# Kernel optimization log

Measured on AMD Instinct MI355X. Metric: run time of the kernel, lower is better.

The kernel has to match this reference:

```python
import jax, jax.numpy as jnp
import numpy as np

SHAPE = (32, 512, 512)  # (D, H, W) dense voxel grid
N_ACTIVE = 150000


def setup_inputs() -> dict:
    key = jax.random.key(0)
    k_f, k_w1, k_w2 = jax.random.split(key, 3)
    D, H, W = SHAPE
    # unique active voxel coordinates (collision-free dense-grid hash)
    rng = np.random.default_rng(0)
    lin = rng.permutation(D * H * W)[:N_ACTIVE]
    z = lin // (H * W)
    y = (lin // W) % H
    x = lin % W
    coors = np.stack([np.zeros(N_ACTIVE, np.int32), z.astype(np.int32),
                      y.astype(np.int32), x.astype(np.int32)], axis=1)
    features = jax.random.normal(k_f, (N_ACTIVE, 3), dtype=jnp.float32)
    # per-offset GEMM weights: [K^3, Cin, Cout]
    w1 = jax.random.normal(k_w1, (27, 3, 128), dtype=jnp.float32) * 0.2
    w2 = jax.random.normal(k_w2, (27, 128, 128), dtype=jnp.float32) * 0.05
    return {"features": features, "coors": jnp.asarray(coors), "w1": w1,
            "w2": w2, "batch_size": 1}


def _build_grid(coors):
    D, H, W = SHAPE
    n = coors.shape[0]
    grid = jnp.full((D, H, W), -1, dtype=jnp.int32)
    return grid.at[coors[:, 1], coors[:, 2], coors[:, 3]].set(
        jnp.arange(n, dtype=jnp.int32))


def _subm_conv3d(feat, coors, grid, w):
    """Submanifold 3x3x3 conv: gather active neighbors per offset, GEMM, accumulate.
    feat: [N, Cin]; w: [27, Cin, Cout]; output defined only on active sites -> [N, Cout]."""
    D, H, W = SHAPE
    n = feat.shape[0]
    out = jnp.zeros((n, w.shape[-1]), dtype=feat.dtype)
    k = 0
    for dz in (-1, 0, 1):
        for dy in (-1, 0, 1):
            for dx in (-1, 0, 1):
                nz = coors[:, 1] + dz
                ny = coors[:, 2] + dy
                nx = coors[:, 3] + dx
                inb = ((nz >= 0) & (nz < D) & (ny >= 0) & (ny < H)
                       & (nx >= 0) & (nx < W))
                nidx = grid[jnp.clip(nz, 0, D - 1), jnp.clip(ny, 0, H - 1),
                            jnp.clip(nx, 0, W - 1)]
                valid = inb & (nidx >= 0)
                g = jnp.where(valid[:, None],
                              feat[jnp.clip(nidx, 0, n - 1)], 0.0)  # [N, Cin]
                out = out + g @ w[k]
                k += 1
    return out


def reference(features, coors, w1, w2, batch_size):
    # SparseConvTensor: features [N,3], coors [N,4] (batch,z,y,x), batch_size=1
    grid = _build_grid(coors)
    h = _subm_conv3d(features, coors, grid, w1)   # SubMConv3d(3, 128, 3)
    out = _subm_conv3d(h, coors, grid, w2)        # SubMConv3d(128, 128, 3), shared indice_key
    return out
```

## Files before the change

kernel.cpp:

```cpp
#include <hip/hip_runtime.h>
#include <stdint.h>

#define GD 32
#define GH 512
#define GW 512
#define GDHW (GD * GH * GW)
#define KOFF 27
#define CAP 4096
#define CNTS 32
#define NW2 (KOFF * 128 * 128)

typedef __attribute__((ext_vector_type(8))) short short8;
typedef __attribute__((ext_vector_type(4))) float f32x4;

__device__ __forceinline__ unsigned short f32_to_bf16(float x) {
    unsigned int u = __float_as_uint(x);
    unsigned int r = (u + 0x7FFFu + ((u >> 16) & 1u)) >> 16;
    return (unsigned short)r;
}

__global__ __launch_bounds__(256) void setup_kernel(
    const int* __restrict__ coors, int* __restrict__ grid,
    const float* __restrict__ w2, unsigned short* __restrict__ w2t,
    int* __restrict__ cnts, int n, int nbsc) {
    const int bid = blockIdx.x, t = threadIdx.x;
    if (bid == 0) {
        for (int q = t; q < 26 * CNTS; q += 256) cnts[q] = 0;
    }
    if (bid < nbsc) {
        int i = bid * 256 + t;
        if (i < n) {
            int z = coors[i * 4 + 1];
            int y = coors[i * 4 + 2];
            int x = coors[i * 4 + 3];
            grid[(z * GH + y) * GW + x] = i;
        }
    } else {
        int g = (bid - nbsc) * 256 + t;
        if (g < NW2) {
            int k = g >> 14;
            int c = (g >> 7) & 127;
            int q = g & 127;
            w2t[g] = f32_to_bf16(w2[(k * 128 + q) * 128 + c]);
        }
    }
}

__global__ __launch_bounds__(256) void nbr_kernel(
    const int* __restrict__ coors, const int* __restrict__ grid,
    int* __restrict__ vcnt, int* __restrict__ nbrc,
    int2* __restrict__ pairs, int* __restrict__ cnts, int n) {
    __shared__ int wcnt[4][26];
    __shared__ int kbase[26];

    const int i = blockIdx.x * 256 + threadIdx.x;
    const int t = threadIdx.x, wave = t >> 6, lane = t & 63;
    const bool live = (i < n);
    const unsigned long long lmask = (1ull << lane) - 1;

    int z = 0, y = 0, x = 0;
    if (live) {
        z = coors[i * 4 + 1];
        y = coors[i * 4 + 2];
        x = coors[i * 4 + 3];
    }

    int j[27];
#pragma unroll
    for (int k = 0; k < 27; ++k) {
        if (k == 13) { j[k] = live ? i : -1; continue; }
        int dz = k / 9 - 1, dy = (k / 3) % 3 - 1, dx = k % 3 - 1;
        int nz = z + dz, ny = y + dy, nx = x + dx;
        int cz = min(max(nz, 0), GD - 1);
        int cy = min(max(ny, 0), GH - 1);
        int cx = min(max(nx, 0), GW - 1);
        int jj = grid[(cz * GH + cy) * GW + cx];
        bool ok = live && nz >= 0 && nz < GD && ny >= 0 && ny < GH &&
                  nx >= 0 && nx < GW;
        j[k] = ok ? jj : -1;
    }

    if (live) {
        int c = 0;
#pragma unroll
        for (int k = 0; k < 27; ++k) {
            if (k == 13) continue;
            if (j[k] >= 0) { nbrc[i * 27 + c] = (k << 20) | j[k]; ++c; }
        }
        vcnt[i] = c;
    }

#pragma unroll
    for (int kk = 0; kk < 26; ++kk) {
        const int k = kk + (kk >= 13);
        unsigned long long m = __ballot(live && (j[k] >= 0));
        if (lane == 0) wcnt[wave][kk] = __popcll(m);
    }
    __syncthreads();
    if (t < 26) {
        int tot = wcnt[0][t] + wcnt[1][t] + wcnt[2][t] + wcnt[3][t];
        kbase[t] = (tot > 0) ? atomicAdd(&cnts[t * CNTS], tot) : 0;
    }
    __syncthreads();
#pragma unroll
    for (int kk = 0; kk < 26; ++kk) {
        const int k = kk + (kk >= 13);
        const bool valid = live && (j[k] >= 0);
        unsigned long long m = __ballot(valid);
        if (valid) {
            int off = 0;
#pragma unroll
            for (int w = 0; w < 4; ++w)
                if (w < wave) off += wcnt[w][kk];
            int pos = kbase[kk] + off + __popcll(m & lmask);
            if (pos < CAP) pairs[kk * CAP + pos] = make_int2(i, j[k]);
        }
    }
}

__global__ __launch_bounds__(256) void conv1_kernel(
    const float* __restrict__ feat, const float* __restrict__ w1,
    const int* __restrict__ vcnt, const int* __restrict__ nbrc,
    unsigned short* __restrict__ hout, int n) {
    const int wave = threadIdx.x >> 6, lane = threadIdx.x & 63;
    const int i = blockIdx.x * 4 + wave;
    if (i >= n) return;
    const int c2 = lane * 2;

    const int cnt = vcnt[i];
    float f0 = feat[i * 3 + 0];
    float f1 = feat[i * 3 + 1];
    float f2 = feat[i * 3 + 2];

    const float* wc = w1 + 13 * 384 + c2;
    float2 w0 = *(const float2*)(wc);
    float2 wv1 = *(const float2*)(wc + 128);
    float2 w2_ = *(const float2*)(wc + 256);
    float a0 = f0 * w0.x + f1 * wv1.x + f2 * w2_.x;
    float a1 = f0 * w0.y + f1 * wv1.y + f2 * w2_.y;

    for (int s = 0; s < cnt; ++s) {
        int e = nbrc[i * 27 + s];
        int k = e >> 20, j = e & 0xFFFFF;
        float g0 = feat[j * 3 + 0];
        float g1 = feat[j * 3 + 1];
        float g2 = feat[j * 3 + 2];
        const float* wk = w1 + k * 384 + c2;
        float2 u0 = *(const float2*)(wk);
        float2 u1 = *(const float2*)(wk + 128);
        float2 u2 = *(const float2*)(wk + 256);
        a0 += g0 * u0.x + g1 * u1.x + g2 * u2.x;
        a1 += g0 * u0.y + g1 * u1.y + g2 * u2.y;
    }

    unsigned int packed = (unsigned int)f32_to_bf16(a0) |
                          ((unsigned int)f32_to_bf16(a1) << 16);
    *(unsigned int*)(hout + (size_t)i * 128 + c2) = packed;
}

__global__ __launch_bounds__(256, 2) void conv2a_kernel(
    const unsigned short* __restrict__ h,
    const unsigned short* __restrict__ w2t,
    float* __restrict__ out, int n) {
    const int t = threadIdx.x;
    const int wave = t >> 6, lane = t & 63;
    const int lane16 = lane & 15, quad = lane >> 4;
    const int wm = wave >> 1, wn = wave & 1;
    const int row0 = blockIdx.x * 128;

    short8 a[4][4];
#pragma unroll
    for (int ms = 0; ms < 4; ++ms) {
        int r = row0 + wm * 64 + ms * 16 + lane16;
        r = min(r, n - 1);
        const unsigned short* hp = h + (size_t)r * 128 + quad * 8;
#pragma unroll
        for (int ks = 0; ks < 4; ++ks)
            a[ms][ks] = *(const short8*)(hp + ks * 32);
    }

    short8 b[4][4];
    const unsigned short* wbase = w2t + 13 * 16384 + quad * 8;
#pragma unroll
    for (int ns = 0; ns < 4; ++ns) {
        int c = wn * 64 + ns * 16 + lane16;
        const unsigned short* wp = wbase + c * 128;
#pragma unroll
        for (int ks = 0; ks < 4; ++ks)
            b[ns][ks] = *(const short8*)(wp + ks * 32);
    }

    f32x4 acc[4][4];
#pragma unroll
    for (int p = 0; p < 4; ++p)
#pragma unroll
        for (int q = 0; q < 4; ++q) acc[p][q] = (f32x4){0.f, 0.f, 0.f, 0.f};

#pragma unroll
    for (int ks = 0; ks < 4; ++ks)
#pragma unroll
        for (int ns = 0; ns < 4; ++ns)
#pragma unroll
            for (int ms = 0; ms < 4; ++ms)
                acc[ms][ns] = __builtin_amdgcn_mfma_f32_16x16x32_bf16(
                    a[ms][ks], b[ns][ks], acc[ms][ns], 0, 0, 0);

#pragma unroll
    for (int ms = 0; ms < 4; ++ms) {
#pragma unroll
        for (int r = 0; r < 4; ++r) {
            int i = row0 + wm * 64 + ms * 16 + quad * 4 + r;
            if (i < n) {
#pragma unroll
                for (int ns = 0; ns < 4; ++ns) {
                    int col = wn * 64 + ns * 16 + lane16;
                    out[(size_t)i * 128 + col] = acc[ms][ns][r];
                }
            }
        }
    }
}

__global__ __launch_bounds__(256, 2) void conv2b_kernel(
    const unsigned short* __restrict__ h,
    const unsigned short* __restrict__ w2t,
    const int2* __restrict__ pairs, const int* __restrict__ cnts,
    float* __restrict__ out) {
    const int kb = blockIdx.x >> 5;
    const int tile = blockIdx.x & 31;
    const int cnt = min(cnts[kb * CNTS], CAP);
    const int base = tile * 128;
    if (base >= cnt) return;
    const int m = min(128, cnt - base);
    const int k = kb + (kb >= 13);
    const int2* pk = pairs + kb * CAP + base;

    const int t = threadIdx.x;
    const int wave = t >> 6, lane = t & 63;
    const int lane16 = lane & 15, quad = lane >> 4;
    const int wm = wave >> 1, wn = wave & 1;

    short8 a[4][4];
#pragma unroll
    for (int ms = 0; ms < 4; ++ms) {
        int r = wm * 64 + ms * 16 + lane16;
        bool v = (r < m);
        int j = v ? pk[r].y : 0;
        const unsigned short* hp = h + (size_t)j * 128 + quad * 8;
#pragma unroll
        for (int ks = 0; ks < 4; ++ks)
            a[ms][ks] = v ? *(const short8*)(hp + ks * 32)
                          : (short8){0, 0, 0, 0, 0, 0, 0, 0};
    }

    short8 b[4][4];
    const unsigned short* wbase = w2t + (size_t)k * 16384 + quad * 8;
#pragma unroll
    for (int ns = 0; ns < 4; ++ns) {
        int c = wn * 64 + ns * 16 + lane16;
        const unsigned short* wp = wbase + c * 128;
#pragma unroll
        for (int ks = 0; ks < 4; ++ks)
            b[ns][ks] = *(const short8*)(wp + ks * 32);
    }

    f32x4 acc[4][4];
#pragma unroll
    for (int p = 0; p < 4; ++p)
#pragma unroll
        for (int q = 0; q < 4; ++q) acc[p][q] = (f32x4){0.f, 0.f, 0.f, 0.f};

#pragma unroll
    for (int ks = 0; ks < 4; ++ks)
#pragma unroll
        for (int ns = 0; ns < 4; ++ns)
#pragma unroll
            for (int ms = 0; ms < 4; ++ms)
                acc[ms][ns] = __builtin_amdgcn_mfma_f32_16x16x32_bf16(
                    a[ms][ks], b[ns][ks], acc[ms][ns], 0, 0, 0);

#pragma unroll
    for (int ms = 0; ms < 4; ++ms) {
#pragma unroll
        for (int r = 0; r < 4; ++r) {
            int row = wm * 64 + ms * 16 + quad * 4 + r;
            if (row < m) {
                int pi = pk[row].x;
#pragma unroll
                for (int ns = 0; ns < 4; ++ns) {
                    int col = wn * 64 + ns * 16 + lane16;
                    unsafeAtomicAdd(&out[(size_t)pi * 128 + col], acc[ms][ns][r]);
                }
            }
        }
    }
}

extern "C" void kernel_launch(void* const* d_in, const int* in_sizes, int n_in,
                              void* d_out, int out_size, void* d_ws,
                              size_t ws_size, hipStream_t stream) {
    const float* feat = (const float*)d_in[0];
    const int* coors = (const int*)d_in[1];
    const float* w1 = (const float*)d_in[2];
    const float* w2 = (const float*)d_in[3];
    float* out = (float*)d_out;

    const int n = in_sizes[0] / 3;

    uint8_t* ws = (uint8_t*)d_ws;
    size_t off = 0;
    int* grid = (int*)(ws + off); off += (size_t)GDHW * 4;
    int* vcnt = (int*)(ws + off); off += (size_t)n * 4;
    int* nbrc = (int*)(ws + off); off += (size_t)n * 27 * 4;
    off = (off + 255) & ~(size_t)255;
    unsigned short* hbuf = (unsigned short*)(ws + off);
    off += (size_t)n * 128 * 2;
    off = (off + 255) & ~(size_t)255;
    unsigned short* w2t = (unsigned short*)(ws + off);
    off += (size_t)KOFF * 128 * 128 * 2;
    off = (off + 255) & ~(size_t)255;
    int2* pairs = (int2*)(ws + off);
    off += (size_t)26 * CAP * sizeof(int2);
    off = (off + 255) & ~(size_t)255;
    int* cnts = (int*)(ws + off); off += 26 * CNTS * 4;

    hipMemsetAsync(grid, 0xFF, (size_t)GDHW * 4, stream);

    const int nbsc = (n + 255) / 256;
    const int nbw2 = (NW2 + 255) / 256;
    setup_kernel<<<nbsc + nbw2, 256, 0, stream>>>(coors, grid, w2, w2t, cnts,
                                                  n, nbsc);
    nbr_kernel<<<nbsc, 256, 0, stream>>>(coors, grid, vcnt, nbrc, pairs, cnts,
                                         n);
    conv1_kernel<<<(n + 3) / 4, 256, 0, stream>>>(feat, w1, vcnt, nbrc, hbuf, n);
    conv2a_kernel<<<(n + 127) / 128, 256, 0, stream>>>(hbuf, w2t, out, n);
    conv2b_kernel<<<26 * 32, 256, 0, stream>>>(hbuf, w2t, pairs, cnts, out);
}
```

Baseline: 241.1 us.

## Replace pair-list scatter conv2 with output-stationary per-offset gather kernel

The neighbor kernel now writes a dense per-offset neighbor index table instead of compacting capped pair lists with block-level ballots and global atomic counters. The two conv2 kernels (centre offset, then a scatter over pair lists with atomic adds into the output) are fused into one output-stationary kernel. Each 128-row tile keeps its accumulators in registers, loops over the 26 offsets, and gathers neighbor rows only for 16-row groups that contain at least one neighbor. This removes the fp32 atomics, the fixed pair capacity and a kernel launch. In exchange it adds a 26×N index table to write and read, and it runs MFMA on sparsely populated 16-row groups.

```diff
diff --git a/kernel.cpp b/kernel.cpp
--- a/kernel.cpp
+++ b/kernel.cpp
@@ -6,8 +6,6 @@
 #define GW 512
 #define GDHW (GD * GH * GW)
 #define KOFF 27
-#define CAP 4096
-#define CNTS 32
 #define NW2 (KOFF * 128 * 128)
 
 typedef __attribute__((ext_vector_type(8))) short short8;
@@ -22,11 +20,8 @@
 __global__ __launch_bounds__(256) void setup_kernel(
     const int* __restrict__ coors, int* __restrict__ grid,
     const float* __restrict__ w2, unsigned short* __restrict__ w2t,
-    int* __restrict__ cnts, int n, int nbsc) {
+    int n, int nbsc) {
     const int bid = blockIdx.x, t = threadIdx.x;
-    if (bid == 0) {
-        for (int q = t; q < 26 * CNTS; q += 256) cnts[q] = 0;
-    }
     if (bid < nbsc) {
         int i = bid * 256 + t;
         if (i < n) {
@@ -49,14 +44,9 @@
 __global__ __launch_bounds__(256) void nbr_kernel(
     const int* __restrict__ coors, const int* __restrict__ grid,
     int* __restrict__ vcnt, int* __restrict__ nbrc,
-    int2* __restrict__ pairs, int* __restrict__ cnts, int n) {
-    __shared__ int wcnt[4][26];
-    __shared__ int kbase[26];
-
+    int* __restrict__ nbk, int n) {
     const int i = blockIdx.x * 256 + threadIdx.x;
-    const int t = threadIdx.x, wave = t >> 6, lane = t & 63;
     const bool live = (i < n);
-    const unsigned long long lmask = (1ull << lane) - 1;
 
     int z = 0, y = 0, x = 0;
     if (live) {
@@ -88,32 +78,10 @@
             if (j[k] >= 0) { nbrc[i * 27 + c] = (k << 20) | j[k]; ++c; }
         }
         vcnt[i] = c;
-    }
-
-#pragma unroll
-    for (int kk = 0; kk < 26; ++kk) {
-        const int k = kk + (kk >= 13);
-        unsigned long long m = __ballot(live && (j[k] >= 0));
-        if (lane == 0) wcnt[wave][kk] = __popcll(m);
-    }
-    __syncthreads();
-    if (t < 26) {
-        int tot = wcnt[0][t] + wcnt[1][t] + wcnt[2][t] + wcnt[3][t];
-        kbase[t] = (tot > 0) ? atomicAdd(&cnts[t * CNTS], tot) : 0;
-    }
-    __syncthreads();
-#pragma unroll
-    for (int kk = 0; kk < 26; ++kk) {
-        const int k = kk + (kk >= 13);
-        const bool valid = live && (j[k] >= 0);
-        unsigned long long m = __ballot(valid);
-        if (valid) {
-            int off = 0;
-#pragma unroll
-            for (int w = 0; w < 4; ++w)
-                if (w < wave) off += wcnt[w][kk];
-            int pos = kbase[kk] + off + __popcll(m & lmask);
-            if (pos < CAP) pairs[kk * CAP + pos] = make_int2(i, j[k]);
+#pragma unroll
+        for (int k = 0; k < 27; ++k) {
+            if (k == 13) continue;
+            nbk[(size_t)k * n + i] = j[k];
         }
     }
 }
@@ -141,10 +109,10 @@
 
     for (int s = 0; s < cnt; ++s) {
         int e = nbrc[i * 27 + s];
-        int k = e >> 20, j = e & 0xFFFFF;
-        float g0 = feat[j * 3 + 0];
-        float g1 = feat[j * 3 + 1];
-        float g2 = feat[j * 3 + 2];
+        int k = e >> 20, jj = e & 0xFFFFF;
+        float g0 = feat[jj * 3 + 0];
+        float g1 = feat[jj * 3 + 1];
+        float g2 = feat[jj * 3 + 2];
         const float* wk = w1 + k * 384 + c2;
         float2 u0 = *(const float2*)(wk);
         float2 u1 = *(const float2*)(wk + 128);
@@ -158,138 +126,106 @@
     *(unsigned int*)(hout + (size_t)i * 128 + c2) = packed;
 }
 
-__global__ __launch_bounds__(256, 2) void conv2a_kernel(
+__global__ __launch_bounds__(256, 2) void conv2_kernel(
     const unsigned short* __restrict__ h,
     const unsigned short* __restrict__ w2t,
+    const int* __restrict__ nbk,
     float* __restrict__ out, int n) {
     const int t = threadIdx.x;
-    const int wave = t >> 6, lane = t & 63;
+    const int lane = t & 63;
     const int lane16 = lane & 15, quad = lane >> 4;
-    const int wm = wave >> 1, wn = wave & 1;
+    const int colbase = (t >> 6) * 32;
     const int row0 = blockIdx.x * 128;
 
-    short8 a[4][4];
-#pragma unroll
-    for (int ms = 0; ms < 4; ++ms) {
-        int r = row0 + wm * 64 + ms * 16 + lane16;
-        r = min(r, n - 1);
-        const unsigned short* hp = h + (size_t)r * 128 + quad * 8;
-#pragma unroll
-        for (int ks = 0; ks < 4; ++ks)
-            a[ms][ks] = *(const short8*)(hp + ks * 32);
-    }
-
-    short8 b[4][4];
-    const unsigned short* wbase = w2t + 13 * 16384 + quad * 8;
-#pragma unroll
-    for (int ns = 0; ns < 4; ++ns) {
-        int c = wn * 64 + ns * 16 + lane16;
-        const unsigned short* wp = wbase + c * 128;
-#pragma unroll
-        for (int ks = 0; ks < 4; ++ks)
-            b[ns][ks] = *(const short8*)(wp + ks * 32);
-    }
-
-    f32x4 acc[4][4];
-#pragma unroll
-    for (int p = 0; p < 4; ++p)
-#pragma unroll
-        for (int q = 0; q < 4; ++q) acc[p][q] = (f32x4){0.f, 0.f, 0.f, 0.f};
-
-#pragma unroll
-    for (int ks = 0; ks < 4; ++ks)
-#pragma unroll
-        for (int ns = 0; ns < 4; ++ns)
-#pragma unroll
-            for (int ms = 0; ms < 4; ++ms)
-                acc[ms][ns] = __builtin_amdgcn_mfma_f32_16x16x32_bf16(
-                    a[ms][ks], b[ns][ks], acc[ms][ns], 0, 0, 0);
-
-#pragma unroll
-    for (int ms = 0; ms < 4; ++ms) {
+    f32x4 acc[8][2];
+#pragma unroll
+    for (int ms = 0; ms < 8; ++ms)
+#pragma unroll
+        for (int ns = 0; ns < 2; ++ns) acc[ms][ns] = (f32x4){0.f, 0.f, 0.f, 0.f};
+
+    {
+        const unsigned short* wb = w2t + 13 * 16384 + quad * 8;
+        short8 b[2][4];
+#pragma unroll
+        for (int ns = 0; ns < 2; ++ns) {
+            const unsigned short* wp = wb + (colbase + ns * 16 + lane16) * 128;
+#pragma unroll
+            for (int ks = 0; ks < 4; ++ks)
+                b[ns][ks] = *(const short8*)(wp + ks * 32);
+        }
+#pragma unroll
+        for (int ms = 0; ms < 8; ++ms) {
+            int r = min(row0 + ms * 16 + lane16, n - 1);
+            const unsigned short* hp = h + (size_t)r * 128 + quad * 8;
+            short8 a[4];
+#pragma unroll
+            for (int ks = 0; ks < 4; ++ks)
+                a[ks] = *(const short8*)(hp + ks * 32);
+#pragma unroll
+            for (int ns = 0; ns < 2; ++ns)
+#pragma unroll
+                for (int ks = 0; ks < 4; ++ks)
+                    acc[ms][ns] = __builtin_amdgcn_mfma_f32_16x16x32_bf16(
+                        a[ks], b[ns][ks], acc[ms][ns], 0, 0, 0);
+        }
+    }
+
+#pragma unroll 1
+    for (int kk = 0; kk < 26; ++kk) {
+        const int k = kk + (kk >= 13);
+        const int* nb = nbk + (size_t)k * n;
+        int r0 = row0 + lane, r1 = row0 + 64 + lane;
+        int j0 = (r0 < n) ? nb[r0] : -1;
+        int j1 = (r1 < n) ? nb[r1] : -1;
+        unsigned long long m0 = __ballot(j0 >= 0);
+        unsigned long long m1 = __ballot(j1 >= 0);
+        if ((m0 | m1) == 0ull) continue;
+
+        const unsigned short* wb = w2t + (size_t)k * 16384 + quad * 8;
+        short8 b[2][4];
+#pragma unroll
+        for (int ns = 0; ns < 2; ++ns) {
+            const unsigned short* wp = wb + (colbase + ns * 16 + lane16) * 128;
+#pragma unroll
+            for (int ks = 0; ks < 4; ++ks)
+                b[ns][ks] = *(const short8*)(wp + ks * 32);
+        }
+
+#pragma unroll
+        for (int ms = 0; ms < 8; ++ms) {
+            unsigned long long msk = (ms < 4) ? m0 : m1;
+            if (((msk >> ((ms & 3) * 16)) & 0xFFFFull) == 0ull)
+                continue;
+            int j = __shfl((ms < 4) ? j0 : j1, (ms & 3) * 16 + lane16);
+            short8 a[4];
+#pragma unroll
+            for (int ks = 0; ks < 4; ++ks)
+                a[ks] = (short8){0, 0, 0, 0, 0, 0, 0, 0};
+            if (j >= 0) {
+                const unsigned short* hp = h + (size_t)j * 128 + quad * 8;
+#pragma unroll
+                for (int ks = 0; ks < 4; ++ks)
+                    a[ks] = *(const short8*)(hp + ks * 32);
+            }
+#pragma unroll
+            for (int ns = 0; ns < 2; ++ns)
+#pragma unroll
+                for (int ks = 0; ks < 4; ++ks)
+                    acc[ms][ns] = __builtin_amdgcn_mfma_f32_16x16x32_bf16(
+                        a[ks], b[ns][ks], acc[ms][ns], 0, 0, 0);
+        }
+    }
+
+#pragma unroll
+    for (int ms = 0; ms < 8; ++ms) {
 #pragma unroll
         for (int r = 0; r < 4; ++r) {
-            int i = row0 + wm * 64 + ms * 16 + quad * 4 + r;
+            int i = row0 + ms * 16 + quad * 4 + r;
             if (i < n) {
 #pragma unroll
-                for (int ns = 0; ns < 4; ++ns) {
-                    int col = wn * 64 + ns * 16 + lane16;
+                for (int ns = 0; ns < 2; ++ns) {
+                    int col = colbase + ns * 16 + lane16;
                     out[(size_t)i * 128 + col] = acc[ms][ns][r];
-                }
-            }
-        }
-    }
-}
-
-__global__ __launch_bounds__(256, 2) void conv2b_kernel(
-    const unsigned short* __restrict__ h,
-    const unsigned short* __restrict__ w2t,
-    const int2* __restrict__ pairs, const int* __restrict__ cnts,
-    float* __restrict__ out) {
-    const int kb = blockIdx.x >> 5;
-    const int tile = blockIdx.x & 31;
-    const int cnt = min(cnts[kb * CNTS], CAP);
-    const int base = tile * 128;
-    if (base >= cnt) return;
-    const int m = min(128, cnt - base);
-    const int k = kb + (kb >= 13);
-    const int2* pk = pairs + kb * CAP + base;
-
-    const int t = threadIdx.x;
-    const int wave = t >> 6, lane = t & 63;
-    const int lane16 = lane & 15, quad = lane >> 4;
-    const int wm = wave >> 1, wn = wave & 1;
-
-    short8 a[4][4];
-#pragma unroll
-    for (int ms = 0; ms < 4; ++ms) {
-        int r = wm * 64 + ms * 16 + lane16;
-        bool v = (r < m);
-        int j = v ? pk[r].y : 0;
-        const unsigned short* hp = h + (size_t)j * 128 + quad * 8;
-#pragma unroll
-        for (int ks = 0; ks < 4; ++ks)
-            a[ms][ks] = v ? *(const short8*)(hp + ks * 32)
-                          : (short8){0, 0, 0, 0, 0, 0, 0, 0};
-    }
-
-    short8 b[4][4];
-    const unsigned short* wbase = w2t + (size_t)k * 16384 + quad * 8;
-#pragma unroll
-    for (int ns = 0; ns < 4; ++ns) {
-        int c = wn * 64 + ns * 16 + lane16;
-        const unsigned short* wp = wbase + c * 128;
-#pragma unroll
-        for (int ks = 0; ks < 4; ++ks)
-            b[ns][ks] = *(const short8*)(wp + ks * 32);
-    }
-
-    f32x4 acc[4][4];
-#pragma unroll
-    for (int p = 0; p < 4; ++p)
-#pragma unroll
-        for (int q = 0; q < 4; ++q) acc[p][q] = (f32x4){0.f, 0.f, 0.f, 0.f};
-
-#pragma unroll
-    for (int ks = 0; ks < 4; ++ks)
-#pragma unroll
-        for (int ns = 0; ns < 4; ++ns)
-#pragma unroll
-            for (int ms = 0; ms < 4; ++ms)
-                acc[ms][ns] = __builtin_amdgcn_mfma_f32_16x16x32_bf16(
-                    a[ms][ks], b[ns][ks], acc[ms][ns], 0, 0, 0);
-
-#pragma unroll
-    for (int ms = 0; ms < 4; ++ms) {
-#pragma unroll
-        for (int r = 0; r < 4; ++r) {
-            int row = wm * 64 + ms * 16 + quad * 4 + r;
-            if (row < m) {
-                int pi = pk[row].x;
-#pragma unroll
-                for (int ns = 0; ns < 4; ++ns) {
-                    int col = wn * 64 + ns * 16 + lane16;
-                    unsafeAtomicAdd(&out[(size_t)pi * 128 + col], acc[ms][ns][r]);
                 }
             }
         }
@@ -312,27 +248,21 @@
     int* grid = (int*)(ws + off); off += (size_t)GDHW * 4;
     int* vcnt = (int*)(ws + off); off += (size_t)n * 4;
     int* nbrc = (int*)(ws + off); off += (size_t)n * 27 * 4;
+    int* nbk  = (int*)(ws + off); off += (size_t)n * 27 * 4;
     off = (off + 255) & ~(size_t)255;
     unsigned short* hbuf = (unsigned short*)(ws + off);
     off += (size_t)n * 128 * 2;
     off = (off + 255) & ~(size_t)255;
     unsigned short* w2t = (unsigned short*)(ws + off);
     off += (size_t)KOFF * 128 * 128 * 2;
-    off = (off + 255) & ~(size_t)255;
-    int2* pairs = (int2*)(ws + off);
-    off += (size_t)26 * CAP * sizeof(int2);
-    off = (off + 255) & ~(size_t)255;
-    int* cnts = (int*)(ws + off); off += 26 * CNTS * 4;
 
     hipMemsetAsync(grid, 0xFF, (size_t)GDHW * 4, stream);
 
     const int nbsc = (n + 255) / 256;
     const int nbw2 = (NW2 + 255) / 256;
-    setup_kernel<<<nbsc + nbw2, 256, 0, stream>>>(coors, grid, w2, w2t, cnts,
-                                                  n, nbsc);
-    nbr_kernel<<<nbsc, 256, 0, stream>>>(coors, grid, vcnt, nbrc, pairs, cnts,
-                                         n);
+    setup_kernel<<<nbsc + nbw2, 256, 0, stream>>>(coors, grid, w2, w2t, n,
+                                                  nbsc);
+    nbr_kernel<<<nbsc, 256, 0, stream>>>(coors, grid, vcnt, nbrc, nbk, n);
     conv1_kernel<<<(n + 3) / 4, 256, 0, stream>>>(feat, w1, vcnt, nbrc, hbuf, n);
-    conv2a_kernel<<<(n + 127) / 128, 256, 0, stream>>>(hbuf, w2t, out, n);
-    conv2b_kernel<<<26 * 32, 256, 0, stream>>>(hbuf, w2t, pairs, cnts, out);
-}
+    conv2_kernel<<<(n + 127) / 128, 256, 0, stream>>>(hbuf, w2t, nbk, out, n);
+}
```

Measured after the change: 354.6 us. +47.1%, slower.

## Replace atomic scatter in neighbor GEMM with bf16 staging buffer and fixup gather

Applied to the files above, without the earlier changes.

The off-center conv2 GEMM now writes its per-pair results as bf16 into a staging buffer instead of doing float atomic adds into the output. A new fixup kernel then walks a compacted list of voxels that have neighbors and gathers their staged contributions into the output. Launch bounds for both conv2 kernels are raised to request higher occupancy. This removes atomic contention but adds extra kernel launches, an extra bf16 round trip that costs some precision, and more index bookkeeping in nbr_kernel.

```diff
diff --git a/kernel.cpp b/kernel.cpp
--- a/kernel.cpp
+++ b/kernel.cpp
@@ -25,7 +25,7 @@
     int* __restrict__ cnts, int n, int nbsc) {
     const int bid = blockIdx.x, t = threadIdx.x;
     if (bid == 0) {
-        for (int q = t; q < 26 * CNTS; q += 256) cnts[q] = 0;
+        for (int q = t; q < 26 * CNTS + 32; q += 256) cnts[q] = 0;
     }
     if (bid < nbsc) {
         int i = bid * 256 + t;
@@ -49,7 +49,9 @@
 __global__ __launch_bounds__(256) void nbr_kernel(
     const int* __restrict__ coors, const int* __restrict__ grid,
     int* __restrict__ vcnt, int* __restrict__ nbrc,
-    int2* __restrict__ pairs, int* __restrict__ cnts, int n) {
+    int* __restrict__ pairs, int* __restrict__ npos,
+    int* __restrict__ cnts, int* __restrict__ rn,
+    int* __restrict__ rlist, int n) {
     __shared__ int wcnt[4][26];
     __shared__ int kbase[26];
 
@@ -80,14 +82,22 @@
         j[k] = ok ? jj : -1;
     }
 
+    int c = 0;
     if (live) {
-        int c = 0;
 #pragma unroll
         for (int k = 0; k < 27; ++k) {
             if (k == 13) continue;
             if (j[k] >= 0) { nbrc[i * 27 + c] = (k << 20) | j[k]; ++c; }
         }
         vcnt[i] = c;
+    }
+
+    {
+        unsigned long long mr = __ballot(live && c > 0);
+        int rbase = 0;
+        if (lane == 0 && mr) rbase = atomicAdd(rn, __popcll(mr));
+        rbase = __shfl(rbase, 0);
+        if (live && c > 0) rlist[rbase + __popcll(mr & lmask)] = i;
     }
 
 #pragma unroll
@@ -102,6 +112,7 @@
         kbase[t] = (tot > 0) ? atomicAdd(&cnts[t * CNTS], tot) : 0;
     }
     __syncthreads();
+    int slot = 0;
 #pragma unroll
     for (int kk = 0; kk < 26; ++kk) {
         const int k = kk + (kk >= 13);
@@ -113,7 +124,13 @@
             for (int w = 0; w < 4; ++w)
                 if (w < wave) off += wcnt[w][kk];
             int pos = kbase[kk] + off + __popcll(m & lmask);
-            if (pos < CAP) pairs[kk * CAP + pos] = make_int2(i, j[k]);
+            if (pos < CAP) {
+                pairs[kk * CAP + pos] = j[k];
+                npos[i * 27 + slot] = kk * CAP + pos;
+            } else {
+                npos[i * 27 + slot] = -1;
+            }
+            ++slot;
         }
     }
 }
@@ -141,10 +158,10 @@
 
     for (int s = 0; s < cnt; ++s) {
         int e = nbrc[i * 27 + s];
-        int k = e >> 20, j = e & 0xFFFFF;
-        float g0 = feat[j * 3 + 0];
-        float g1 = feat[j * 3 + 1];
-        float g2 = feat[j * 3 + 2];
+        int k = e >> 20, jj = e & 0xFFFFF;
+        float g0 = feat[jj * 3 + 0];
+        float g1 = feat[jj * 3 + 1];
+        float g2 = feat[jj * 3 + 2];
         const float* wk = w1 + k * 384 + c2;
         float2 u0 = *(const float2*)(wk);
         float2 u1 = *(const float2*)(wk + 128);
@@ -158,7 +175,7 @@
     *(unsigned int*)(hout + (size_t)i * 128 + c2) = packed;
 }
 
-__global__ __launch_bounds__(256, 2) void conv2a_kernel(
+__global__ __launch_bounds__(256, 4) void conv2a_kernel(
     const unsigned short* __restrict__ h,
     const unsigned short* __restrict__ w2t,
     float* __restrict__ out, int n) {
@@ -221,11 +238,11 @@
     }
 }
 
-__global__ __launch_bounds__(256, 2) void conv2b_kernel(
+__global__ __launch_bounds__(256, 4) void conv2b_kernel(
     const unsigned short* __restrict__ h,
     const unsigned short* __restrict__ w2t,
-    const int2* __restrict__ pairs, const int* __restrict__ cnts,
-    float* __restrict__ out) {
+    const int* __restrict__ pairs, const int* __restrict__ cnts,
+    unsigned short* __restrict__ corr) {
     const int kb = blockIdx.x >> 5;
     const int tile = blockIdx.x & 31;
     const int cnt = min(cnts[kb * CNTS], CAP);
@@ -233,7 +250,7 @@
     if (base >= cnt) return;
     const int m = min(128, cnt - base);
     const int k = kb + (kb >= 13);
-    const int2* pk = pairs + kb * CAP + base;
+    const int* pk = pairs + kb * CAP + base;
 
     const int t = threadIdx.x;
     const int wave = t >> 6, lane = t & 63;
@@ -245,7 +262,7 @@
     for (int ms = 0; ms < 4; ++ms) {
         int r = wm * 64 + ms * 16 + lane16;
         bool v = (r < m);
-        int j = v ? pk[r].y : 0;
+        int j = v ? pk[r] : 0;
         const unsigned short* hp = h + (size_t)j * 128 + quad * 8;
 #pragma unroll
         for (int ks = 0; ks < 4; ++ks)
@@ -285,15 +302,44 @@
         for (int r = 0; r < 4; ++r) {
             int row = wm * 64 + ms * 16 + quad * 4 + r;
             if (row < m) {
-                int pi = pk[row].x;
+                unsigned short* cr =
+                    corr + (size_t)(kb * CAP + base + row) * 128;
 #pragma unroll
                 for (int ns = 0; ns < 4; ++ns) {
                     int col = wn * 64 + ns * 16 + lane16;
-                    unsafeAtomicAdd(&out[(size_t)pi * 128 + col], acc[ms][ns][r]);
+                    cr[col] = f32_to_bf16(acc[ms][ns][r]);
                 }
             }
         }
     }
+}
+
+__global__ __launch_bounds__(256) void fixup_kernel(
+    const unsigned short* __restrict__ corr, const int* __restrict__ vcnt,
+    const int* __restrict__ npos, const int* __restrict__ rlist,
+    const int* __restrict__ rn, float* __restrict__ out) {
+    const int widx = blockIdx.x * 4 + (threadIdx.x >> 6);
+    const int lane = threadIdx.x & 63;
+    if (widx >= rn[0]) return;
+    const int i = rlist[widx];
+    const int cnt = vcnt[i];
+    const int* np = npos + i * 27;
+
+    float a0 = 0.f, a1 = 0.f;
+    for (int s = 0; s < cnt; ++s) {
+        int p = np[s];
+        if (p >= 0) {
+            unsigned int u =
+                *(const unsigned int*)(corr + (size_t)p * 128 + lane * 2);
+            a0 += __uint_as_float(u << 16);
+            a1 += __uint_as_float(u & 0xFFFF0000u);
+        }
+    }
+    float2* op = (float2*)(out + (size_t)i * 128) + lane;
+    float2 cur = *op;
+    cur.x += a0;
+    cur.y += a1;
+    *op = cur;
 }
 
 extern "C" void kernel_launch(void* const* d_in, const int* in_sizes, int n_in,
@@ -312,6 +358,8 @@
     int* grid = (int*)(ws + off); off += (size_t)GDHW * 4;
     int* vcnt = (int*)(ws + off); off += (size_t)n * 4;
     int* nbrc = (int*)(ws + off); off += (size_t)n * 27 * 4;
+    int* npos = (int*)(ws + off); off += (size_t)n * 27 * 4;
+    int* rlist = (int*)(ws + off); off += (size_t)n * 4;
     off = (off + 255) & ~(size_t)255;
     unsigned short* hbuf = (unsigned short*)(ws + off);
     off += (size_t)n * 128 * 2;
@@ -319,10 +367,14 @@
     unsigned short* w2t = (unsigned short*)(ws + off);
     off += (size_t)KOFF * 128 * 128 * 2;
     off = (off + 255) & ~(size_t)255;
-    int2* pairs = (int2*)(ws + off);
-    off += (size_t)26 * CAP * sizeof(int2);
-    off = (off + 255) & ~(size_t)255;
-    int* cnts = (int*)(ws + off); off += 26 * CNTS * 4;
+    int* pairs = (int*)(ws + off);
+    off += (size_t)26 * CAP * 4;
+    off = (off + 255) & ~(size_t)255;
+    int* cnts = (int*)(ws + off); off += (26 * CNTS + 32) * 4;
+    int* rn = cnts + 26 * CNTS;
+    off = (off + 255) & ~(size_t)255;
+    unsigned short* corr = (unsigned short*)(ws + off);
+    off += (size_t)26 * CAP * 128 * 2;
 
     hipMemsetAsync(grid, 0xFF, (size_t)GDHW * 4, stream);
 
@@ -330,9 +382,11 @@
     const int nbw2 = (NW2 + 255) / 256;
     setup_kernel<<<nbsc + nbw2, 256, 0, stream>>>(coors, grid, w2, w2t, cnts,
                                                   n, nbsc);
-    nbr_kernel<<<nbsc, 256, 0, stream>>>(coors, grid, vcnt, nbrc, pairs, cnts,
-                                         n);
+    nbr_kernel<<<nbsc, 256, 0, stream>>>(coors, grid, vcnt, nbrc, pairs, npos,
+                                         cnts, rn, rlist, n);
     conv1_kernel<<<(n + 3) / 4, 256, 0, stream>>>(feat, w1, vcnt, nbrc, hbuf, n);
+    conv2b_kernel<<<26 * 32, 256, 0, stream>>>(hbuf, w2t, pairs, cnts, corr);
     conv2a_kernel<<<(n + 127) / 128, 256, 0, stream>>>(hbuf, w2t, out, n);
-    conv2b_kernel<<<26 * 32, 256, 0, stream>>>(hbuf, w2t, pairs, cnts, out);
-}
+    fixup_kernel<<<(n + 3) / 4, 256, 0, stream>>>(corr, vcnt, npos, rlist, rn,
+                                                  out);
+}
```

Result: slower. 263.1 us (+9.1%).
